# Optimization experiments

Hardware: AMD Instinct MI355X
Metric: run time of the kernel (lower is better)

## Reference

```python
import jax, jax.numpy as jnp
import numpy as np

B, N, D, K = 1024, 8192, 256, 8
LAMBDA_MULT = 0.01

def setup_inputs() -> dict:
    key = jax.random.key(0)
    k1, k2, k3, k4, k5 = jax.random.split(key, 5)
    x = jax.random.uniform(k1, (B, D), dtype=jnp.float32)
    mu = jax.random.uniform(k2, (N, D), dtype=jnp.float32)
    lambda_base = jax.random.uniform(k3, (N,), dtype=jnp.float32) * LAMBDA_MULT
    v = jax.random.normal(k4, (N, K, D), dtype=jnp.float32)  # stands in for per-unit orthogonal init
    omega = 0.1 + 0.4 * jax.random.uniform(k5, (N, K), dtype=jnp.float32)
    return {"x": x, "mu": mu, "lambda_base": lambda_base, "v": v, "omega": omega}

def reference(x, mu, lambda_base, v, omega):
    # quad_form = diff^T (lambda*I + sum_k omega_k v_k v_k^T) diff
    #           = lambda * ||x - mu||^2 + sum_k omega_k * ((x - mu) . v_k)^2
    # Woodbury-style expansion avoids materializing W:(n,d,d) and diff:(b,n,d).
    x2 = jnp.sum(x * x, axis=-1)                      # (b,)
    mu2 = jnp.sum(mu * mu, axis=-1)                   # (n,)
    xm = x @ mu.T                                     # (b,n)
    sqdist = x2[:, None] - 2.0 * xm + mu2[None, :]    # (b,n) = ||x-mu||^2
    xv = jnp.einsum('bd,nkd->bnk', x, v)              # (b,n,k)
    muv = jnp.einsum('nd,nkd->nk', mu, v)             # (n,k)
    proj2 = (xv - muv[None, :, :]) ** 2               # (b,n,k)
    quad = lambda_base[None, :] * sqdist + jnp.einsum('bnk,nk->bn', proj2, omega)
    return jnp.exp(-quad / D)  # Type == 'exp'
```

## Files before the change

### kernel.cpp

```cpp
#include <hip/hip_runtime.h>


#define B_SZ 1024
#define N_SZ 8192
#define D_SZ 256
#define K_SZ 8

#define BT 128
#define NT 16

typedef __bf16 bf16x8 __attribute__((ext_vector_type(8)));
typedef float f32x4 __attribute__((ext_vector_type(4)));
typedef unsigned short u16x4 __attribute__((ext_vector_type(4)));
typedef unsigned short u16x8 __attribute__((ext_vector_type(8)));

#define WS_X2   0u
#define WS_MU2  4096u
#define WS_MUV  36864u
#define WS_PX   299008u
#define WS_PW   823296u
#define WS_NEED (823296ull + 37748736ull)

__device__ __forceinline__ float wave_reduce(float s) {
#pragma unroll
  for (int off = 32; off > 0; off >>= 1) s += __shfl_down(s, off);
  return s;
}

__device__ __forceinline__ u16x4 cvt4(float4 t) {
  u16x4 r;
  r[0] = __builtin_bit_cast(unsigned short, (__bf16)t.x);
  r[1] = __builtin_bit_cast(unsigned short, (__bf16)t.y);
  r[2] = __builtin_bit_cast(unsigned short, (__bf16)t.z);
  r[3] = __builtin_bit_cast(unsigned short, (__bf16)t.w);
  return r;
}

__device__ __forceinline__ void glds16(const void* g, const void* l) {
  __builtin_amdgcn_global_load_lds(
      (const __attribute__((address_space(1))) void*)g,
      (__attribute__((address_space(3))) void*)l, 16, 0, 0);
}

__global__ void prep_x(const float* __restrict__ x, float* __restrict__ x2,
                       unsigned short* __restrict__ px) {
  const int w = threadIdx.x >> 6, lane = threadIdx.x & 63;
  const int b = blockIdx.x * 4 + w;
  float4 t = *(const float4*)(x + (size_t)b * D_SZ + 4 * lane);
  *(u16x4*)(px + (size_t)b * D_SZ + 4 * lane) = cvt4(t);
  float s = t.x * t.x + t.y * t.y + t.z * t.z + t.w * t.w;
  s = wave_reduce(s);
  if (lane == 0) x2[b] = s;
}

__global__ void prep_w(const float* __restrict__ mu, const float* __restrict__ v,
                       float* __restrict__ mu2, float* __restrict__ muv,
                       unsigned short* __restrict__ pw) {
  __shared__ __align__(16) float mulds[D_SZ];
  const int n = blockIdx.x;
  const int w = threadIdx.x >> 6, lane = threadIdx.x & 63;
  if (w == 0) {
    float4 m4 = *(const float4*)(mu + (size_t)n * D_SZ + 4 * lane);
    *(float4*)(mulds + 4 * lane) = m4;
    *(u16x4*)(pw + (size_t)n * 9 * D_SZ + 4 * lane) = cvt4(m4);
    float s = m4.x * m4.x + m4.y * m4.y + m4.z * m4.z + m4.w * m4.w;
    s = wave_reduce(s);
    if (lane == 0) mu2[n] = s;
  }
  __syncthreads();
  float4 m4 = *(const float4*)(mulds + 4 * lane);
#pragma unroll
  for (int kk = 0; kk < 2; ++kk) {
    const int k = w * 2 + kk;
    float4 v4 = *(const float4*)(v + ((size_t)n * K_SZ + k) * D_SZ + 4 * lane);
    *(u16x4*)(pw + ((size_t)n * 9 + k + 1) * D_SZ + 4 * lane) = cvt4(v4);
    float s = m4.x * v4.x + m4.y * v4.y + m4.z * v4.z + m4.w * v4.w;
    s = wave_reduce(s);
    if (lane == 0) muv[n * K_SZ + k] = s;
  }
}

__global__ __launch_bounds__(256, 2)
void hmu_main_p(const unsigned short* __restrict__ px,
                const unsigned short* __restrict__ pw,
                const float* __restrict__ lam, const float* __restrict__ om,
                const float* __restrict__ wsf, float* __restrict__ out) {
  __shared__ __align__(16) unsigned short As[BT * 32];
  __shared__ __align__(16) unsigned short Bs[NT * 9 * 32];

  const float* ws_x2 = wsf;
  const float* ws_mu2 = wsf + 1024;
  const float* ws_muv = wsf + 9216;

  const int tid = threadIdx.x;
  const int lane = tid & 63;
  const int w = tid >> 6;
  const int m = lane & 15;
  const int kg = lane >> 4;
  const int nl4 = lane >> 2;
  const int ch = lane & 3;

  const int n0 = blockIdx.x * NT;
  const int b0 = blockIdx.y * BT;

  f32x4 acc[2][9];
#pragma unroll
  for (int bs = 0; bs < 2; ++bs)
#pragma unroll
    for (int j = 0; j < 9; ++j) acc[bs][j] = (f32x4){0.f, 0.f, 0.f, 0.f};

  for (int kt = 0; kt < 8; ++kt) {
    const int k0 = kt * 32;
#pragma unroll
    for (int t = 0; t < 2; ++t) {
      int r0 = w * 32 + t * 16;
      glds16(px + (size_t)(b0 + r0 + nl4) * D_SZ + k0 + ch * 8, As + r0 * 32);
    }
#pragma unroll
    for (int t = 0; t < 3; ++t) {
      int i = w + 4 * t;
      if (i < 9)
        glds16(pw + ((size_t)(n0 + nl4) * 9 + i) * D_SZ + k0 + ch * 8,
               Bs + i * 16 * 32);
    }
    __syncthreads();

    bf16x8 af[2];
#pragma unroll
    for (int bs = 0; bs < 2; ++bs)
      af[bs] = *(const bf16x8*)&As[((2 * w + bs) * 16 + m) * 32 + kg * 8];
#pragma unroll
    for (int j = 0; j < 9; ++j) {
      bf16x8 bfr = *(const bf16x8*)&Bs[(j * 16 + m) * 32 + kg * 8];
      acc[0][j] = __builtin_amdgcn_mfma_f32_16x16x32_bf16(af[0], bfr, acc[0][j], 0, 0, 0);
      acc[1][j] = __builtin_amdgcn_mfma_f32_16x16x32_bf16(af[1], bfr, acc[1][j], 0, 0, 0);
    }
    __syncthreads();
  }

  const int n = n0 + m;
  const float lam_n = lam[n];
  const float mu2_n = ws_mu2[n];
  float omr[8], muvr[8];
#pragma unroll
  for (int k = 0; k < 8; ++k) {
    omr[k] = om[n * 8 + k];
    muvr[k] = ws_muv[n * 8 + k];
  }
#pragma unroll
  for (int bs = 0; bs < 2; ++bs) {
#pragma unroll
    for (int r = 0; r < 4; ++r) {
      int b = b0 + (2 * w + bs) * 16 + kg * 4 + r;
      float x2b = ws_x2[b];
      float c0 = acc[bs][0][r];
      float q = lam_n * (x2b - 2.f * c0 + mu2_n);
#pragma unroll
      for (int k = 0; k < 8; ++k) {
        float p = acc[bs][k + 1][r] - muvr[k];
        q = fmaf(omr[k] * p, p, q);
      }
      out[(size_t)b * N_SZ + n] = __expf(q * (-1.0f / 256.0f));
    }
  }
}

__device__ __forceinline__ void cvt16_store(const float* __restrict__ src,
                                            unsigned short* dst) {
  const float4* p4 = (const float4*)src;
  float fv[16];
#pragma unroll
  for (int e = 0; e < 4; ++e) {
    float4 t = p4[e];
    fv[4 * e + 0] = t.x; fv[4 * e + 1] = t.y;
    fv[4 * e + 2] = t.z; fv[4 * e + 3] = t.w;
  }
  u16x8 lo, hi;
#pragma unroll
  for (int e = 0; e < 8; ++e) {
    lo[e] = __builtin_bit_cast(unsigned short, (__bf16)fv[e]);
    hi[e] = __builtin_bit_cast(unsigned short, (__bf16)fv[e + 8]);
  }
  *(u16x8*)dst = lo;
  *(u16x8*)(dst + 8) = hi;
}

#define LDS_STRIDE 40
__global__ __launch_bounds__(256, 2)
void hmu_main_f(const float* __restrict__ x, const float* __restrict__ mu,
                const float* __restrict__ lam, const float* __restrict__ v,
                const float* __restrict__ om, const float* __restrict__ ws,
                float* __restrict__ out) {
  __shared__ __align__(16) unsigned short As[BT * LDS_STRIDE];
  __shared__ __align__(16) unsigned short Bs[NT * 9 * LDS_STRIDE];
  const float* ws_x2 = ws;
  const float* ws_mu2 = ws + 1024;
  const float* ws_muv = ws + 9216;
  const int tid = threadIdx.x, lane = tid & 63, w = tid >> 6;
  const int m = lane & 15, kg = lane >> 4;
  const int n0 = blockIdx.x * NT, b0 = blockIdx.y * BT;
  f32x4 acc[2][9];
#pragma unroll
  for (int bs = 0; bs < 2; ++bs)
#pragma unroll
    for (int j = 0; j < 9; ++j) acc[bs][j] = (f32x4){0.f, 0.f, 0.f, 0.f};
  const int arow = tid >> 1, ahalf = tid & 1;
  for (int kt = 0; kt < 8; ++kt) {
    const int k0 = kt * 32;
    cvt16_store(x + (size_t)(b0 + arow) * D_SZ + k0 + ahalf * 16,
                &As[arow * LDS_STRIDE + ahalf * 16]);
#pragma unroll
    for (int it = 0; it < 2; ++it) {
      int idx = tid + 256 * it;
      if (idx < 288) {
        int row = idx >> 1, half = idx & 1;
        int nl = row / 9, j = row - nl * 9;
        const float* src = (j == 0)
            ? mu + (size_t)(n0 + nl) * D_SZ + k0 + half * 16
            : v + (size_t)((n0 + nl) * K_SZ + (j - 1)) * D_SZ + k0 + half * 16;
        cvt16_store(src, &Bs[row * LDS_STRIDE + half * 16]);
      }
    }
    __syncthreads();
    bf16x8 af[2];
#pragma unroll
    for (int bs = 0; bs < 2; ++bs)
      af[bs] = *(const bf16x8*)&As[((2 * w + bs) * 16 + m) * LDS_STRIDE + kg * 8];
#pragma unroll
    for (int j = 0; j < 9; ++j) {
      bf16x8 bfr = *(const bf16x8*)&Bs[(m * 9 + j) * LDS_STRIDE + kg * 8];
      acc[0][j] = __builtin_amdgcn_mfma_f32_16x16x32_bf16(af[0], bfr, acc[0][j], 0, 0, 0);
      acc[1][j] = __builtin_amdgcn_mfma_f32_16x16x32_bf16(af[1], bfr, acc[1][j], 0, 0, 0);
    }
    __syncthreads();
  }
  const int n = n0 + m;
  const float lam_n = lam[n];
  const float mu2_n = ws_mu2[n];
  float omr[8], muvr[8];
#pragma unroll
  for (int k = 0; k < 8; ++k) {
    omr[k] = om[n * 8 + k];
    muvr[k] = ws_muv[n * 8 + k];
  }
#pragma unroll
  for (int bs = 0; bs < 2; ++bs)
#pragma unroll
    for (int r = 0; r < 4; ++r) {
      int b = b0 + (2 * w + bs) * 16 + kg * 4 + r;
      float c0 = acc[bs][0][r];
      float q = lam_n * (ws_x2[b] - 2.f * c0 + mu2_n);
#pragma unroll
      for (int k = 0; k < 8; ++k) {
        float p = acc[bs][k + 1][r] - muvr[k];
        q = fmaf(omr[k] * p, p, q);
      }
      out[(size_t)b * N_SZ + n] = __expf(q * (-1.0f / 256.0f));
    }
}

__global__ void p2_mu_f(const float* __restrict__ mu, const float* __restrict__ v,
                        float* __restrict__ mu2, float* __restrict__ muv) {
  __shared__ __align__(16) float mulds[D_SZ];
  const int n = blockIdx.x;
  const int w = threadIdx.x >> 6, lane = threadIdx.x & 63;
  if (w == 0) {
    float4 m4 = *(const float4*)(mu + (size_t)n * D_SZ + 4 * lane);
    *(float4*)(mulds + 4 * lane) = m4;
    float s = m4.x * m4.x + m4.y * m4.y + m4.z * m4.z + m4.w * m4.w;
    s = wave_reduce(s);
    if (lane == 0) mu2[n] = s;
  }
  __syncthreads();
  float4 m4 = *(const float4*)(mulds + 4 * lane);
#pragma unroll
  for (int kk = 0; kk < 2; ++kk) {
    const int k = w * 2 + kk;
    float4 v4 = *(const float4*)(v + ((size_t)n * K_SZ + k) * D_SZ + 4 * lane);
    float s = m4.x * v4.x + m4.y * v4.y + m4.z * v4.z + m4.w * v4.w;
    s = wave_reduce(s);
    if (lane == 0) muv[n * K_SZ + k] = s;
  }
}

__global__ void p1_x2_f(const float* __restrict__ x, float* __restrict__ x2) {
  const int w = threadIdx.x >> 6, lane = threadIdx.x & 63;
  const int b = blockIdx.x * 4 + w;
  float4 t = *(const float4*)(x + (size_t)b * D_SZ + 4 * lane);
  float s = t.x * t.x + t.y * t.y + t.z * t.z + t.w * t.w;
  s = wave_reduce(s);
  if (lane == 0) x2[b] = s;
}

extern "C" void kernel_launch(void* const* d_in, const int* in_sizes, int n_in,
                              void* d_out, int out_size, void* d_ws, size_t ws_size,
                              hipStream_t stream) {
  const float* x   = (const float*)d_in[0];
  const float* mu  = (const float*)d_in[1];
  const float* lam = (const float*)d_in[2];
  const float* v   = (const float*)d_in[3];
  const float* om  = (const float*)d_in[4];
  float* out = (float*)d_out;
  char* wsb = (char*)d_ws;
  float* wsf = (float*)d_ws;
  float* x2  = (float*)(wsb + WS_X2);
  float* mu2 = (float*)(wsb + WS_MU2);
  float* muv = (float*)(wsb + WS_MUV);

  dim3 grid(N_SZ / NT, B_SZ / BT);
  if (ws_size >= WS_NEED) {
    unsigned short* px = (unsigned short*)(wsb + WS_PX);
    unsigned short* pw = (unsigned short*)(wsb + WS_PW);
    prep_x<<<B_SZ / 4, 256, 0, stream>>>(x, x2, px);
    prep_w<<<N_SZ, 256, 0, stream>>>(mu, v, mu2, muv, pw);
    hmu_main_p<<<grid, 256, 0, stream>>>(px, pw, lam, om, wsf, out);
  } else {
    p1_x2_f<<<B_SZ / 4, 256, 0, stream>>>(x, x2);
    p2_mu_f<<<N_SZ, 256, 0, stream>>>(mu, v, mu2, muv);
    hmu_main_f<<<grid, 256, 0, stream>>>(x, mu, lam, v, om, wsf, out);
  }
}
```

Measured before the change: 172.1 us.

## Pre-pack operands into MFMA fragment layout and double batch tile to 256

The prep kernels now write x and the mu/v weights into a tile-major packed bf16 layout that matches the MFMA fragment order. Each main-kernel k-step then loads contiguous 1 KB chunks with global_load_lds, and the LDS reads become conflict-free. The batch tile grows from 128 to 256, so each wave computes 4x9 accumulators and every B fragment is reused across four A fragments, halving the weight reloads per output. The cost is more accumulator registers (144 floats), which may hurt occupancy under launch_bounds(256,2), and prep_w now processes 16 units per block with serialized per-k barriers.

```diff
diff --git a/kernel.cpp b/kernel.cpp
--- a/kernel.cpp
+++ b/kernel.cpp
@@ -6,13 +6,13 @@
 #define D_SZ 256
 #define K_SZ 8
 
-#define BT 128
+#define BT 256
 #define NT 16
 
 typedef __bf16 bf16x8 __attribute__((ext_vector_type(8)));
 typedef float f32x4 __attribute__((ext_vector_type(4)));
-typedef unsigned short u16x4 __attribute__((ext_vector_type(4)));
 typedef unsigned short u16x8 __attribute__((ext_vector_type(8)));
+typedef unsigned short ushort_t;
 
 #define WS_X2   0u
 #define WS_MU2  4096u
@@ -27,66 +27,118 @@
   return s;
 }
 
-__device__ __forceinline__ u16x4 cvt4(float4 t) {
-  u16x4 r;
-  r[0] = __builtin_bit_cast(unsigned short, (__bf16)t.x);
-  r[1] = __builtin_bit_cast(unsigned short, (__bf16)t.y);
-  r[2] = __builtin_bit_cast(unsigned short, (__bf16)t.z);
-  r[3] = __builtin_bit_cast(unsigned short, (__bf16)t.w);
-  return r;
-}
-
 __device__ __forceinline__ void glds16(const void* g, const void* l) {
   __builtin_amdgcn_global_load_lds(
       (const __attribute__((address_space(1))) void*)g,
       (__attribute__((address_space(3))) void*)l, 16, 0, 0);
 }
 
+__device__ __forceinline__ u16x8 cvt8(const float* sp) {
+  u16x8 o;
+#pragma unroll
+  for (int e = 0; e < 8; ++e)
+    o[e] = __builtin_bit_cast(unsigned short, (__bf16)sp[e]);
+  return o;
+}
+
 __global__ void prep_x(const float* __restrict__ x, float* __restrict__ x2,
-                       unsigned short* __restrict__ px) {
-  const int w = threadIdx.x >> 6, lane = threadIdx.x & 63;
-  const int b = blockIdx.x * 4 + w;
-  float4 t = *(const float4*)(x + (size_t)b * D_SZ + 4 * lane);
-  *(u16x4*)(px + (size_t)b * D_SZ + 4 * lane) = cvt4(t);
-  float s = t.x * t.x + t.y * t.y + t.z * t.z + t.w * t.w;
-  s = wave_reduce(s);
-  if (lane == 0) x2[b] = s;
+                       ushort_t* __restrict__ px_p) {
+  __shared__ float xl[16 * 260];
+  const int g = blockIdx.x, t = threadIdx.x;
+  const int r = t >> 4, c16 = t & 15;
+  {
+    const float* src = x + ((size_t)(g * 16 + r)) * D_SZ + c16 * 16;
+#pragma unroll
+    for (int i = 0; i < 4; ++i)
+      *(float4*)(xl + r * 260 + c16 * 16 + 4 * i) = *(const float4*)(src + 4 * i);
+  }
+  __syncthreads();
+  const int w = t >> 6, lane = t & 63;
+#pragma unroll
+  for (int rr = 0; rr < 4; ++rr) {
+    int row = w * 4 + rr;
+    const float* rp = xl + row * 260 + lane * 4;
+    float s = rp[0] * rp[0] + rp[1] * rp[1] + rp[2] * rp[2] + rp[3] * rp[3];
+    s = wave_reduce(s);
+    if (lane == 0) x2[g * 16 + row] = s;
+  }
+#pragma unroll
+  for (int i = 0; i < 2; ++i) {
+    int q = t + 256 * i;
+    int kt = q >> 6, slot = q & 63;
+    int c = slot >> 4, rw = slot & 15;
+    const float* sp = xl + rw * 260 + kt * 32 + c * 8;
+    *(u16x8*)(px_p + (((size_t)g * 8 + kt) * 64 + slot) * 8) = cvt8(sp);
+  }
 }
 
 __global__ void prep_w(const float* __restrict__ mu, const float* __restrict__ v,
                        float* __restrict__ mu2, float* __restrict__ muv,
-                       unsigned short* __restrict__ pw) {
-  __shared__ __align__(16) float mulds[D_SZ];
-  const int n = blockIdx.x;
-  const int w = threadIdx.x >> 6, lane = threadIdx.x & 63;
-  if (w == 0) {
-    float4 m4 = *(const float4*)(mu + (size_t)n * D_SZ + 4 * lane);
-    *(float4*)(mulds + 4 * lane) = m4;
-    *(u16x4*)(pw + (size_t)n * 9 * D_SZ + 4 * lane) = cvt4(m4);
-    float s = m4.x * m4.x + m4.y * m4.y + m4.z * m4.z + m4.w * m4.w;
+                       ushort_t* __restrict__ pw_p) {
+  __shared__ float muL[16 * 260];
+  __shared__ float vL[16 * 260];
+  const int ng = blockIdx.x, t = threadIdx.x;
+  const int r = t >> 4, c16 = t & 15;
+  const int w = t >> 6, lane = t & 63;
+  {
+    const float* src = mu + ((size_t)(ng * 16 + r)) * D_SZ + c16 * 16;
+#pragma unroll
+    for (int i = 0; i < 4; ++i)
+      *(float4*)(muL + r * 260 + c16 * 16 + 4 * i) = *(const float4*)(src + 4 * i);
+  }
+  __syncthreads();
+#pragma unroll
+  for (int rr = 0; rr < 4; ++rr) {
+    int row = w * 4 + rr;
+    const float* rp = muL + row * 260 + lane * 4;
+    float s = rp[0] * rp[0] + rp[1] * rp[1] + rp[2] * rp[2] + rp[3] * rp[3];
     s = wave_reduce(s);
-    if (lane == 0) mu2[n] = s;
-  }
-  __syncthreads();
-  float4 m4 = *(const float4*)(mulds + 4 * lane);
-#pragma unroll
-  for (int kk = 0; kk < 2; ++kk) {
-    const int k = w * 2 + kk;
-    float4 v4 = *(const float4*)(v + ((size_t)n * K_SZ + k) * D_SZ + 4 * lane);
-    *(u16x4*)(pw + ((size_t)n * 9 + k + 1) * D_SZ + 4 * lane) = cvt4(v4);
-    float s = m4.x * v4.x + m4.y * v4.y + m4.z * v4.z + m4.w * v4.w;
-    s = wave_reduce(s);
-    if (lane == 0) muv[n * K_SZ + k] = s;
+    if (lane == 0) mu2[ng * 16 + row] = s;
+  }
+#pragma unroll
+  for (int i = 0; i < 2; ++i) {
+    int q = t + 256 * i;
+    int kt = q >> 6, slot = q & 63;
+    int c = slot >> 4, rw = slot & 15;
+    const float* sp = muL + rw * 260 + kt * 32 + c * 8;
+    *(u16x8*)(pw_p + ((((size_t)ng * 9 + 0) * 8 + kt) * 64 + slot) * 8) = cvt8(sp);
+  }
+  for (int j = 1; j <= 8; ++j) {
+    __syncthreads();
+    {
+      const float* src = v + (((size_t)(ng * 16 + r)) * K_SZ + (j - 1)) * D_SZ + c16 * 16;
+#pragma unroll
+      for (int i = 0; i < 4; ++i)
+        *(float4*)(vL + r * 260 + c16 * 16 + 4 * i) = *(const float4*)(src + 4 * i);
+    }
+    __syncthreads();
+#pragma unroll
+    for (int rr = 0; rr < 4; ++rr) {
+      int row = w * 4 + rr;
+      const float* ap = muL + row * 260 + lane * 4;
+      const float* bp = vL + row * 260 + lane * 4;
+      float s = ap[0] * bp[0] + ap[1] * bp[1] + ap[2] * bp[2] + ap[3] * bp[3];
+      s = wave_reduce(s);
+      if (lane == 0) muv[(ng * 16 + row) * K_SZ + (j - 1)] = s;
+    }
+#pragma unroll
+    for (int i = 0; i < 2; ++i) {
+      int q = t + 256 * i;
+      int kt = q >> 6, slot = q & 63;
+      int c = slot >> 4, rw = slot & 15;
+      const float* sp = vL + rw * 260 + kt * 32 + c * 8;
+      *(u16x8*)(pw_p + ((((size_t)ng * 9 + j) * 8 + kt) * 64 + slot) * 8) = cvt8(sp);
+    }
   }
 }
 
 __global__ __launch_bounds__(256, 2)
-void hmu_main_p(const unsigned short* __restrict__ px,
-                const unsigned short* __restrict__ pw,
+void hmu_main_p(const ushort_t* __restrict__ px_p,
+                const ushort_t* __restrict__ pw_p,
                 const float* __restrict__ lam, const float* __restrict__ om,
                 const float* __restrict__ wsf, float* __restrict__ out) {
-  __shared__ __align__(16) unsigned short As[BT * 32];
-  __shared__ __align__(16) unsigned short Bs[NT * 9 * 32];
+  __shared__ __align__(16) ushort_t As[16 * 512];
+  __shared__ __align__(16) ushort_t Bs[9 * 512];
 
   const float* ws_x2 = wsf;
   const float* ws_mu2 = wsf + 1024;
@@ -97,43 +149,40 @@
   const int w = tid >> 6;
   const int m = lane & 15;
   const int kg = lane >> 4;
-  const int nl4 = lane >> 2;
-  const int ch = lane & 3;
-
-  const int n0 = blockIdx.x * NT;
+
+  const int ng = blockIdx.x;
+  const int n0 = ng * NT;
+  const int g0 = blockIdx.y * 16;
   const int b0 = blockIdx.y * BT;
 
-  f32x4 acc[2][9];
-#pragma unroll
-  for (int bs = 0; bs < 2; ++bs)
+  f32x4 acc[4][9];
+#pragma unroll
+  for (int bs = 0; bs < 4; ++bs)
 #pragma unroll
     for (int j = 0; j < 9; ++j) acc[bs][j] = (f32x4){0.f, 0.f, 0.f, 0.f};
 
   for (int kt = 0; kt < 8; ++kt) {
-    const int k0 = kt * 32;
-#pragma unroll
-    for (int t = 0; t < 2; ++t) {
-      int r0 = w * 32 + t * 16;
-      glds16(px + (size_t)(b0 + r0 + nl4) * D_SZ + k0 + ch * 8, As + r0 * 32);
-    }
-#pragma unroll
-    for (int t = 0; t < 3; ++t) {
-      int i = w + 4 * t;
-      if (i < 9)
-        glds16(pw + ((size_t)(n0 + nl4) * 9 + i) * D_SZ + k0 + ch * 8,
-               Bs + i * 16 * 32);
-    }
-    __syncthreads();
-
-    bf16x8 af[2];
-#pragma unroll
-    for (int bs = 0; bs < 2; ++bs)
-      af[bs] = *(const bf16x8*)&As[((2 * w + bs) * 16 + m) * 32 + kg * 8];
+#pragma unroll
+    for (int tt = 0; tt < 4; ++tt) {
+      int gl = w * 4 + tt;
+      glds16(px_p + (((size_t)(g0 + gl) * 8 + kt) * 64 + lane) * 8, As + gl * 512);
+    }
+    glds16(pw_p + ((((size_t)ng * 9 + w) * 8 + kt) * 64 + lane) * 8, Bs + w * 512);
+    glds16(pw_p + ((((size_t)ng * 9 + w + 4) * 8 + kt) * 64 + lane) * 8, Bs + (w + 4) * 512);
+    if (w == 0)
+      glds16(pw_p + ((((size_t)ng * 9 + 8) * 8 + kt) * 64 + lane) * 8, Bs + 8 * 512);
+    __syncthreads();
+
+    bf16x8 af[4];
+#pragma unroll
+    for (int bs = 0; bs < 4; ++bs)
+      af[bs] = *(const bf16x8*)&As[(w * 4 + bs) * 512 + (kg * 16 + m) * 8];
 #pragma unroll
     for (int j = 0; j < 9; ++j) {
-      bf16x8 bfr = *(const bf16x8*)&Bs[(j * 16 + m) * 32 + kg * 8];
-      acc[0][j] = __builtin_amdgcn_mfma_f32_16x16x32_bf16(af[0], bfr, acc[0][j], 0, 0, 0);
-      acc[1][j] = __builtin_amdgcn_mfma_f32_16x16x32_bf16(af[1], bfr, acc[1][j], 0, 0, 0);
+      bf16x8 bfr = *(const bf16x8*)&Bs[j * 512 + (kg * 16 + m) * 8];
+#pragma unroll
+      for (int bs = 0; bs < 4; ++bs)
+        acc[bs][j] = __builtin_amdgcn_mfma_f32_16x16x32_bf16(af[bs], bfr, acc[bs][j], 0, 0, 0);
     }
     __syncthreads();
   }
@@ -148,10 +197,10 @@
     muvr[k] = ws_muv[n * 8 + k];
   }
 #pragma unroll
-  for (int bs = 0; bs < 2; ++bs) {
+  for (int bs = 0; bs < 4; ++bs) {
 #pragma unroll
     for (int r = 0; r < 4; ++r) {
-      int b = b0 + (2 * w + bs) * 16 + kg * 4 + r;
+      int b = b0 + (w * 4 + bs) * 16 + kg * 4 + r;
       float x2b = ws_x2[b];
       float c0 = acc[bs][0][r];
       float q = lam_n * (x2b - 2.f * c0 + mu2_n);
@@ -165,6 +214,8 @@
   }
 }
 
+typedef unsigned short u16x4 __attribute__((ext_vector_type(4)));
+
 __device__ __forceinline__ void cvt16_store(const float* __restrict__ src,
                                             unsigned short* dst) {
   const float4* p4 = (const float4*)src;
@@ -186,19 +237,20 @@
 }
 
 #define LDS_STRIDE 40
+#define FBT 128
 __global__ __launch_bounds__(256, 2)
 void hmu_main_f(const float* __restrict__ x, const float* __restrict__ mu,
                 const float* __restrict__ lam, const float* __restrict__ v,
                 const float* __restrict__ om, const float* __restrict__ ws,
                 float* __restrict__ out) {
-  __shared__ __align__(16) unsigned short As[BT * LDS_STRIDE];
+  __shared__ __align__(16) unsigned short As[FBT * LDS_STRIDE];
   __shared__ __align__(16) unsigned short Bs[NT * 9 * LDS_STRIDE];
   const float* ws_x2 = ws;
   const float* ws_mu2 = ws + 1024;
   const float* ws_muv = ws + 9216;
   const int tid = threadIdx.x, lane = tid & 63, w = tid >> 6;
   const int m = lane & 15, kg = lane >> 4;
-  const int n0 = blockIdx.x * NT, b0 = blockIdx.y * BT;
+  const int n0 = blockIdx.x * NT, b0 = blockIdx.y * FBT;
   f32x4 acc[2][9];
 #pragma unroll
   for (int bs = 0; bs < 2; ++bs)
@@ -307,16 +359,17 @@
   float* mu2 = (float*)(wsb + WS_MU2);
   float* muv = (float*)(wsb + WS_MUV);
 
-  dim3 grid(N_SZ / NT, B_SZ / BT);
   if (ws_size >= WS_NEED) {
-    unsigned short* px = (unsigned short*)(wsb + WS_PX);
-    unsigned short* pw = (unsigned short*)(wsb + WS_PW);
-    prep_x<<<B_SZ / 4, 256, 0, stream>>>(x, x2, px);
-    prep_w<<<N_SZ, 256, 0, stream>>>(mu, v, mu2, muv, pw);
-    hmu_main_p<<<grid, 256, 0, stream>>>(px, pw, lam, om, wsf, out);
+    ushort_t* px_p = (ushort_t*)(wsb + WS_PX);
+    ushort_t* pw_p = (ushort_t*)(wsb + WS_PW);
+    prep_x<<<B_SZ / 16, 256, 0, stream>>>(x, x2, px_p);
+    prep_w<<<N_SZ / 16, 256, 0, stream>>>(mu, v, mu2, muv, pw_p);
+    dim3 grid(N_SZ / NT, B_SZ / BT);
+    hmu_main_p<<<grid, 256, 0, stream>>>(px_p, pw_p, lam, om, wsf, out);
   } else {
     p1_x2_f<<<B_SZ / 4, 256, 0, stream>>>(x, x2);
     p2_mu_f<<<N_SZ, 256, 0, stream>>>(mu, v, mu2, muv);
+    dim3 grid(N_SZ / NT, B_SZ / FBT);
     hmu_main_f<<<grid, 256, 0, stream>>>(x, mu, lam, v, om, wsf, out);
   }
 }
```

After: 213.6 us. 24.2% more time.
